# Kernel optimization log

Measured on AMD Instinct MI355X. Metric: run time of the kernel, lower is better.

The kernel has to match this reference:

```python
import jax, jax.numpy as jnp
import numpy as np

CURVATURE = -1.0
BN_EPS = 1e-5


def setup_inputs() -> dict:
    key = jax.random.key(0)
    k1, k2, k3 = jax.random.split(key, 3)
    B, Q, D, O = 4, 256, 256, 256  # Q must equal O for torch BatchNorm1d on 3D input
    x = jax.random.normal(k1, (B, Q, D), dtype=jnp.float32)
    # kaiming_uniform_(a=sqrt(5)) -> bound = 1/sqrt(fan_in)
    b_lc = 1.0 / np.sqrt(D * D)
    lc_w = jax.random.uniform(k2, (O, D, D), dtype=jnp.float32, minval=-b_lc, maxval=b_lc)
    b_w1 = 1.0 / np.sqrt(D)
    w1 = jax.random.uniform(k3, (O, D), dtype=jnp.float32, minval=-b_w1, maxval=b_w1)
    bias = jnp.zeros((O,), dtype=jnp.float32)
    gamma = jnp.ones((O,), dtype=jnp.float32)   # BN weight (channels = dim 1 = Q == O)
    beta = jnp.zeros((O,), dtype=jnp.float32)   # BN bias
    return {"x": x, "lc_w": lc_w, "w1": w1, "bias": bias, "gamma": gamma, "beta": beta}


def reference(x, lc_w, w1, bias, gamma, beta):
    B, Q, D = x.shape
    O = lc_w.shape[0]
    # pairwise products P[b,q,j,k] = x_j * x_k  (computed ONCE, shared across all i)
    P = x[:, :, :, None] * x[:, :, None, :]                     # [B,Q,D,D]
    # denom[b,j,k] = 1 + c * ||x[:,:,j]*x[:,:,k]||_2^2 over the query dim (dim=1)
    denom = 1.0 + CURVATURE * jnp.einsum('bqjk,bqjk->bjk', P, P)  # [B,D,D]
    # mask diagonal j==k in the weights (cheaper than masking P)
    mask = 1.0 - jnp.eye(D, dtype=x.dtype)
    Wm = lc_w * mask                                             # [O,D,D]
    lc_out = jnp.einsum('bqjk,ijk->bqi', P / denom[:, None, :, :], Wm)  # [B,Q,O]
    base = jnp.einsum('bqd,od->bqo', x, w1) + bias               # F.linear
    y = lc_out + base                                            # [B,Q,O]
    # BatchNorm1d(out_features) on 3D input: channels are dim 1 (requires Q == O),
    # training-mode batch stats over dims (0, 2), biased variance.
    mean = jnp.mean(y, axis=(0, 2), keepdims=True)
    var = jnp.mean((y - mean) ** 2, axis=(0, 2), keepdims=True)
    y_hat = (y - mean) / jnp.sqrt(var + BN_EPS)
    out = gamma[None, :, None] * y_hat + beta[None, :, None]
    # dropout treated as identity (eval mode) for a deterministic reference
    return out
```

## Files before the change

### kernel.cpp

```cpp
#include <hip/hip_runtime.h>
#include <hip/hip_bf16.h>

typedef __attribute__((ext_vector_type(8))) short short8;
typedef __attribute__((ext_vector_type(4))) float f32x4;
typedef __attribute__((ext_vector_type(4))) unsigned int u32x4;

#define LDP 40

static __device__ __forceinline__ unsigned int cvt_pk_bf16(float lo, float hi) {
    unsigned int r;
    asm("v_cvt_pk_bf16_f32 %0, %1, %2" : "=v"(r) : "v"(lo), "v"(hi));
    return r;
}

__global__ __launch_bounds__(256) void k_wcvt(const float* __restrict__ W,
                                              const float* __restrict__ w1,
                                              unsigned short* __restrict__ Wbf,
                                              unsigned short* __restrict__ w1bf) {
    long t0 = (long)blockIdx.x * 256 + threadIdx.x;
    for (long u = t0; u < 2097152L; u += 524288L) {
        long i = u >> 13;
        int uu = (int)(u & 8191);
        int c = uu >> 2, cu = uu & 3;
        int s = (int)((i >> 1) & 3);
        const float* src = W + i * 65536 + c * 32 + (cu ^ s) * 8;
        f32x4 a = *(const f32x4*)src;
        f32x4 b = *(const f32x4*)(src + 4);
        u32x4 q;
        q.x = cvt_pk_bf16(a.x, a.y); q.y = cvt_pk_bf16(a.z, a.w);
        q.z = cvt_pk_bf16(b.x, b.y); q.w = cvt_pk_bf16(b.z, b.w);
        *(u32x4*)(Wbf + u * 8) = q;
    }
    if (t0 < 8192) {
        long u = t0;
        long i = u >> 5;
        int uu = (int)(u & 31);
        int c = uu >> 2, cu = uu & 3;
        int s = (int)((i >> 1) & 3);
        const float* src = w1 + i * 256 + c * 32 + (cu ^ s) * 8;
        f32x4 a = *(const f32x4*)src;
        f32x4 b = *(const f32x4*)(src + 4);
        u32x4 q;
        q.x = cvt_pk_bf16(a.x, a.y); q.y = cvt_pk_bf16(a.z, a.w);
        q.z = cvt_pk_bf16(b.x, b.y); q.w = cvt_pk_bf16(b.z, b.w);
        *(u32x4*)(w1bf + u * 8) = q;
    }
}

__global__ __launch_bounds__(256) void k_pre(const float* __restrict__ x,
                                             float* __restrict__ T) {
    int bid = blockIdx.x, t = threadIdx.x;
    int b = bid >> 6;
    int j4 = (bid & 63) * 4;
    const float* xb = x + (long)b * 65536;
    float ac0 = 0.f, ac1 = 0.f, ac2 = 0.f, ac3 = 0.f;
    #pragma unroll 8
    for (int qq = 0; qq < 256; ++qq) {
        const float* row = xb + (long)qq * 256;
        float xk = row[t];
        float xk2 = xk * xk;
        f32x4 aj = *(const f32x4*)(row + j4);
        ac0 = fmaf(aj.x * aj.x, xk2, ac0);
        ac1 = fmaf(aj.y * aj.y, xk2, ac1);
        ac2 = fmaf(aj.z * aj.z, xk2, ac2);
        ac3 = fmaf(aj.w * aj.w, xk2, ac3);
    }
    long base = (long)b * 65536 + (long)j4 * 256 + t;
    T[base +   0] = (j4     == t) ? 0.f : 1.f / (1.f - ac0);
    T[base + 256] = (j4 + 1 == t) ? 0.f : 1.f / (1.f - ac1);
    T[base + 512] = (j4 + 2 == t) ? 0.f : 1.f / (1.f - ac2);
    T[base + 768] = (j4 + 3 == t) ? 0.f : 1.f / (1.f - ac3);
}

__global__ __launch_bounds__(256, 3) void k_gemm(const float* __restrict__ x,
                                                 const unsigned short* __restrict__ Wbf,
                                                 const unsigned short* __restrict__ w1bf,
                                                 const float* __restrict__ T,
                                                 float* __restrict__ partials) {
    __shared__ unsigned short As[2][128][LDP];
    __shared__ unsigned short Bs[2][128][32];

    const int bid = blockIdx.x;
    const int mt = bid >> 6;
    const int nt = (bid >> 5) & 1;
    const int sp = bid & 31;
    const int tid = threadIdx.x;
    const int lane = tid & 63;
    const int l15 = lane & 15;
    const int cu = lane >> 4;
    const int xu = cu ^ ((l15 >> 1) & 3);
    const int wid = tid >> 6;
    const int wm = wid >> 1, wn = wid & 1;
    const int b = mt >> 1;

    const int r = tid >> 1;
    const int ch = (tid & 1) * 16;

    const float* xrow = x + (long)(mt * 128 + r) * 256;
    const float* Trow = T + (long)b * 65536 + (long)(sp * 8) * 256 + ch;

    const unsigned short* Bsrc0 = Wbf + (long)(nt * 128 + wid * 32 + (lane >> 2)) * 65536
                                      + (long)sp * 2048 + (lane & 3) * 8;
    const unsigned short* Bsrc1 = Bsrc0 + 16L * 65536;

    f32x4 xjA = *(const f32x4*)(xrow + sp * 8);
    f32x4 xjB = *(const f32x4*)(xrow + sp * 8 + 4);
    const float xj8[8] = {xjA.x, xjA.y, xjA.z, xjA.w, xjB.x, xjB.y, xjB.z, xjB.w};

    f32x4 acc[4][4];
    #pragma unroll
    for (int a = 0; a < 4; ++a)
        #pragma unroll
        for (int c = 0; c < 4; ++c) acc[a][c] = (f32x4){0.f, 0.f, 0.f, 0.f};

    f32x4 xw0, xw1, xw2, xw3;

    {
        __builtin_amdgcn_global_load_lds(
            (const __attribute__((address_space(1))) unsigned int*)Bsrc0,
            (__attribute__((address_space(3))) unsigned int*)&Bs[0][wid * 32][0], 16, 0, 0);
        __builtin_amdgcn_global_load_lds(
            (const __attribute__((address_space(1))) unsigned int*)Bsrc1,
            (__attribute__((address_space(3))) unsigned int*)&Bs[0][wid * 32 + 16][0], 16, 0, 0);
        xw0 = *(const f32x4*)(xrow + ch + 0);
        xw1 = *(const f32x4*)(xrow + ch + 4);
        xw2 = *(const f32x4*)(xrow + ch + 8);
        xw3 = *(const f32x4*)(xrow + ch + 12);
        f32x4 t0 = *(const f32x4*)(Trow + 0);
        f32x4 t1 = *(const f32x4*)(Trow + 4);
        f32x4 t2 = *(const f32x4*)(Trow + 8);
        f32x4 t3 = *(const f32x4*)(Trow + 12);
        const float xj = xj8[0];
        u32x4 qa, qb;
        qa.x = cvt_pk_bf16(xj * xw0.x * t0.x, xj * xw0.y * t0.y);
        qa.y = cvt_pk_bf16(xj * xw0.z * t0.z, xj * xw0.w * t0.w);
        qa.z = cvt_pk_bf16(xj * xw1.x * t1.x, xj * xw1.y * t1.y);
        qa.w = cvt_pk_bf16(xj * xw1.z * t1.z, xj * xw1.w * t1.w);
        qb.x = cvt_pk_bf16(xj * xw2.x * t2.x, xj * xw2.y * t2.y);
        qb.y = cvt_pk_bf16(xj * xw2.z * t2.z, xj * xw2.w * t2.w);
        qb.z = cvt_pk_bf16(xj * xw3.x * t3.x, xj * xw3.y * t3.y);
        qb.w = cvt_pk_bf16(xj * xw3.z * t3.z, xj * xw3.w * t3.w);
        *(u32x4*)&As[0][r][ch]     = qa;
        *(u32x4*)&As[0][r][ch + 8] = qb;
    }
    __syncthreads();

    #pragma unroll 1
    for (int kw = 0; kw < 8; ++kw) {
        #pragma unroll
        for (int jj = 0; jj < 8; ++jj) {
            const int buf = jj & 1;
            const int nbuf = buf ^ 1;
            const int njj = (jj + 1) & 7;
            const int nkw = (jj == 7) ? kw + 1 : kw;
            const bool last = (jj == 7) && (kw == 7);

            f32x4 t0, t1, t2, t3;
            f32x4 nx0 = xw0, nx1 = xw1, nx2 = xw2, nx3 = xw3;
            if (!last) {
                const long noff = (long)njj * 256 + (long)nkw * 32;
                __builtin_amdgcn_global_load_lds(
                    (const __attribute__((address_space(1))) unsigned int*)(Bsrc0 + noff),
                    (__attribute__((address_space(3))) unsigned int*)&Bs[nbuf][wid * 32][0], 16, 0, 0);
                __builtin_amdgcn_global_load_lds(
                    (const __attribute__((address_space(1))) unsigned int*)(Bsrc1 + noff),
                    (__attribute__((address_space(3))) unsigned int*)&Bs[nbuf][wid * 32 + 16][0], 16, 0, 0);
                t0 = *(const f32x4*)(Trow + noff + 0);
                t1 = *(const f32x4*)(Trow + noff + 4);
                t2 = *(const f32x4*)(Trow + noff + 8);
                t3 = *(const f32x4*)(Trow + noff + 12);
                if (jj == 7) {
                    const long xo = (long)(kw + 1) * 32;
                    nx0 = *(const f32x4*)(xrow + xo + ch + 0);
                    nx1 = *(const f32x4*)(xrow + xo + ch + 4);
                    nx2 = *(const f32x4*)(xrow + xo + ch + 8);
                    nx3 = *(const f32x4*)(xrow + xo + ch + 12);
                }
            }

            short8 af[4], bfv[4];
            #pragma unroll
            for (int mf = 0; mf < 4; ++mf)
                af[mf] = *(const short8*)&As[buf][wm * 64 + mf * 16 + l15][cu * 8];
            #pragma unroll
            for (int nf = 0; nf < 4; ++nf)
                bfv[nf] = *(const short8*)((const char*)(&Bs[buf][0][0])
                            + (wn * 64 + nf * 16 + l15) * 64 + xu * 16);
            #pragma unroll
            for (int mf = 0; mf < 4; ++mf)
                #pragma unroll
                for (int nf = 0; nf < 4; ++nf)
                    acc[mf][nf] = __builtin_amdgcn_mfma_f32_16x16x32_bf16(
                        af[mf], bfv[nf], acc[mf][nf], 0, 0, 0);

            if (!last) {
                const float xjn = xj8[njj];
                u32x4 qa, qb;
                qa.x = cvt_pk_bf16(xjn * nx0.x * t0.x, xjn * nx0.y * t0.y);
                qa.y = cvt_pk_bf16(xjn * nx0.z * t0.z, xjn * nx0.w * t0.w);
                qa.z = cvt_pk_bf16(xjn * nx1.x * t1.x, xjn * nx1.y * t1.y);
                qa.w = cvt_pk_bf16(xjn * nx1.z * t1.z, xjn * nx1.w * t1.w);
                qb.x = cvt_pk_bf16(xjn * nx2.x * t2.x, xjn * nx2.y * t2.y);
                qb.y = cvt_pk_bf16(xjn * nx2.z * t2.z, xjn * nx2.w * t2.w);
                qb.z = cvt_pk_bf16(xjn * nx3.x * t3.x, xjn * nx3.y * t3.y);
                qb.w = cvt_pk_bf16(xjn * nx3.z * t3.z, xjn * nx3.w * t3.w);
                *(u32x4*)&As[nbuf][r][ch]     = qa;
                *(u32x4*)&As[nbuf][r][ch + 8] = qb;
            }
            __syncthreads();
            if (jj == 7) { xw0 = nx0; xw1 = nx1; xw2 = nx2; xw3 = nx3; }
        }
    }

    if (sp < 8) {
        const unsigned short* W1s = w1bf + (long)(nt * 128 + wid * 32 + (lane >> 2)) * 256
                                        + sp * 32 + (lane & 3) * 8;
        __builtin_amdgcn_global_load_lds(
            (const __attribute__((address_space(1))) unsigned int*)W1s,
            (__attribute__((address_space(3))) unsigned int*)&Bs[0][wid * 32][0], 16, 0, 0);
        __builtin_amdgcn_global_load_lds(
            (const __attribute__((address_space(1))) unsigned int*)(W1s + 16L * 256),
            (__attribute__((address_space(3))) unsigned int*)&Bs[0][wid * 32 + 16][0], 16, 0, 0);
        f32x4 a0 = *(const f32x4*)(xrow + sp * 32 + ch + 0);
        f32x4 a1 = *(const f32x4*)(xrow + sp * 32 + ch + 4);
        f32x4 a2 = *(const f32x4*)(xrow + sp * 32 + ch + 8);
        f32x4 a3 = *(const f32x4*)(xrow + sp * 32 + ch + 12);
        u32x4 qa, qb;
        qa.x = cvt_pk_bf16(a0.x, a0.y); qa.y = cvt_pk_bf16(a0.z, a0.w);
        qa.z = cvt_pk_bf16(a1.x, a1.y); qa.w = cvt_pk_bf16(a1.z, a1.w);
        qb.x = cvt_pk_bf16(a2.x, a2.y); qb.y = cvt_pk_bf16(a2.z, a2.w);
        qb.z = cvt_pk_bf16(a3.x, a3.y); qb.w = cvt_pk_bf16(a3.z, a3.w);
        *(u32x4*)&As[0][r][ch]     = qa;
        *(u32x4*)&As[0][r][ch + 8] = qb;
        __syncthreads();
        short8 af[4], bfv[4];
        #pragma unroll
        for (int mf = 0; mf < 4; ++mf)
            af[mf] = *(const short8*)&As[0][wm * 64 + mf * 16 + l15][cu * 8];
        #pragma unroll
        for (int nf = 0; nf < 4; ++nf)
            bfv[nf] = *(const short8*)((const char*)(&Bs[0][0][0])
                        + (wn * 64 + nf * 16 + l15) * 64 + xu * 16);
        #pragma unroll
        for (int mf = 0; mf < 4; ++mf)
            #pragma unroll
            for (int nf = 0; nf < 4; ++nf)
                acc[mf][nf] = __builtin_amdgcn_mfma_f32_16x16x32_bf16(
                    af[mf], bfv[nf], acc[mf][nf], 0, 0, 0);
    }

    float* Pp = partials + (long)sp * 262144;
    #pragma unroll
    for (int mf = 0; mf < 4; ++mf) {
        int rowb = mt * 128 + wm * 64 + mf * 16 + (lane >> 4) * 4;
        #pragma unroll
        for (int nf = 0; nf < 4; ++nf) {
            int col = nt * 128 + wn * 64 + nf * 16 + l15;
            #pragma unroll
            for (int rr = 0; rr < 4; ++rr)
                Pp[(long)(rowb + rr) * 256 + col] = acc[mf][nf][rr];
        }
    }
}

__global__ __launch_bounds__(256) void k_sum(const float* __restrict__ partials,
                                             const float* __restrict__ bias,
                                             float* __restrict__ y,
                                             float2* __restrict__ bstats) {
    int m = blockIdx.x;
    int o = threadIdx.x;
    float acc = bias[o];
    #pragma unroll 8
    for (int spi = 0; spi < 32; ++spi)
        acc += partials[((long)spi * 1024 + m) * 256 + o];
    y[(long)m * 256 + o] = acc;

    float s = acc, s2 = acc * acc;
    #pragma unroll
    for (int off = 32; off > 0; off >>= 1) {
        s  += __shfl_down(s, off, 64);
        s2 += __shfl_down(s2, off, 64);
    }
    __shared__ float rs[4], rq[4];
    int lane = o & 63, wv = o >> 6;
    if (lane == 0) { rs[wv] = s; rq[wv] = s2; }
    __syncthreads();
    if (o == 0) {
        float2 st;
        st.x = rs[0] + rs[1] + rs[2] + rs[3];
        st.y = rq[0] + rq[1] + rq[2] + rq[3];
        bstats[m] = st;
    }
}

__global__ __launch_bounds__(256) void k_bn(const float* __restrict__ y,
                                            const float2* __restrict__ bstats,
                                            const float* __restrict__ gamma,
                                            const float* __restrict__ beta,
                                            float* __restrict__ out) {
    int m = blockIdx.x;
    int o = threadIdx.x;
    int q = m & 255;
    float2 s0 = bstats[q], s1 = bstats[256 + q], s2 = bstats[512 + q], s3 = bstats[768 + q];
    float ts = s0.x + s1.x + s2.x + s3.x;
    float tq = s0.y + s1.y + s2.y + s3.y;
    float mean = ts * (1.f / 1024.f);
    float var = tq * (1.f / 1024.f) - mean * mean;
    float rstd = rsqrtf(var + 1e-5f);
    float v = y[(long)m * 256 + o];
    out[(long)m * 256 + o] = fmaf((v - mean) * rstd, gamma[q], beta[q]);
}

extern "C" void kernel_launch(void* const* d_in, const int* in_sizes, int n_in,
                              void* d_out, int out_size, void* d_ws, size_t ws_size,
                              hipStream_t stream) {
    const float* x     = (const float*)d_in[0];
    const float* lc_w  = (const float*)d_in[1];
    const float* w1    = (const float*)d_in[2];
    const float* bias  = (const float*)d_in[3];
    const float* gamma = (const float*)d_in[4];
    const float* beta  = (const float*)d_in[5];
    float* out = (float*)d_out;

    char* ws = (char*)d_ws;
    size_t o_T     = 0;
    size_t o_part  = o_T + 1048576;
    size_t o_y     = o_part + 33554432;
    size_t o_bst   = o_y + 1048576;
    size_t o_Wbf   = o_bst + 8192;
    size_t o_w1bf  = o_Wbf + 33554432;

    float*          T        = (float*)(ws + o_T);
    float*          partials = (float*)(ws + o_part);
    float*          y        = (float*)(ws + o_y);
    float2*         bstats   = (float2*)(ws + o_bst);
    unsigned short* Wbf      = (unsigned short*)(ws + o_Wbf);
    unsigned short* w1bf     = (unsigned short*)(ws + o_w1bf);

    k_wcvt<<<2048, 256, 0, stream>>>(lc_w, w1, Wbf, w1bf);
    k_pre <<<256,  256, 0, stream>>>(x, T);
    k_gemm<<<512,  256, 0, stream>>>(x, Wbf, w1bf, T, partials);
    k_sum <<<1024, 256, 0, stream>>>(partials, bias, y, bstats);
    k_bn  <<<1024, 256, 0, stream>>>(y, bstats, gamma, beta, out);
}
```

Baseline: 204.8 us.

## Triple-buffer B tiles with vmcnt-based barriers, swizzle A in LDS, merge prep kernels

The GEMM main loop now prefetches B tiles two steps ahead into a three-slot LDS ring. It replaces __syncthreads with a partial s_waitcnt vmcnt barrier so global-to-LDS loads stay in flight across iterations. The A tile drops its padded stride in favour of an XOR swizzle matching the read pattern, and the T scale loads are software-pipelined one step ahead. The weight-conversion and denominator kernels are fused into one launch, and the GEMM's launch bounds drop to two blocks per CU, which risks lower occupancy in exchange for more registers.

```diff
diff --git a/kernel.cpp b/kernel.cpp
--- a/kernel.cpp
+++ b/kernel.cpp
@@ -4,8 +4,6 @@
 typedef __attribute__((ext_vector_type(8))) short short8;
 typedef __attribute__((ext_vector_type(4))) float f32x4;
 typedef __attribute__((ext_vector_type(4))) unsigned int u32x4;
-
-#define LDP 40
 
 static __device__ __forceinline__ unsigned int cvt_pk_bf16(float lo, float hi) {
     unsigned int r;
@@ -13,72 +11,84 @@
     return r;
 }
 
-__global__ __launch_bounds__(256) void k_wcvt(const float* __restrict__ W,
+#define GLDS(src, dst) __builtin_amdgcn_global_load_lds( \
+    (const __attribute__((address_space(1))) unsigned int*)(src), \
+    (__attribute__((address_space(3))) unsigned int*)(dst), 16, 0, 0)
+
+#define BARC(N) do { \
+    asm volatile("s_waitcnt lgkmcnt(0) vmcnt(" #N ")" ::: "memory"); \
+    __builtin_amdgcn_s_barrier(); \
+    __builtin_amdgcn_sched_barrier(0); \
+} while (0)
+
+__global__ __launch_bounds__(256) void k_prep(const float* __restrict__ x,
+                                              const float* __restrict__ W,
                                               const float* __restrict__ w1,
                                               unsigned short* __restrict__ Wbf,
-                                              unsigned short* __restrict__ w1bf) {
-    long t0 = (long)blockIdx.x * 256 + threadIdx.x;
-    for (long u = t0; u < 2097152L; u += 524288L) {
-        long i = u >> 13;
-        int uu = (int)(u & 8191);
-        int c = uu >> 2, cu = uu & 3;
-        int s = (int)((i >> 1) & 3);
-        const float* src = W + i * 65536 + c * 32 + (cu ^ s) * 8;
-        f32x4 a = *(const f32x4*)src;
-        f32x4 b = *(const f32x4*)(src + 4);
-        u32x4 q;
-        q.x = cvt_pk_bf16(a.x, a.y); q.y = cvt_pk_bf16(a.z, a.w);
-        q.z = cvt_pk_bf16(b.x, b.y); q.w = cvt_pk_bf16(b.z, b.w);
-        *(u32x4*)(Wbf + u * 8) = q;
-    }
-    if (t0 < 8192) {
-        long u = t0;
-        long i = u >> 5;
-        int uu = (int)(u & 31);
-        int c = uu >> 2, cu = uu & 3;
-        int s = (int)((i >> 1) & 3);
-        const float* src = w1 + i * 256 + c * 32 + (cu ^ s) * 8;
-        f32x4 a = *(const f32x4*)src;
-        f32x4 b = *(const f32x4*)(src + 4);
-        u32x4 q;
-        q.x = cvt_pk_bf16(a.x, a.y); q.y = cvt_pk_bf16(a.z, a.w);
-        q.z = cvt_pk_bf16(b.x, b.y); q.w = cvt_pk_bf16(b.z, b.w);
-        *(u32x4*)(w1bf + u * 8) = q;
-    }
-}
-
-__global__ __launch_bounds__(256) void k_pre(const float* __restrict__ x,
-                                             float* __restrict__ T) {
+                                              unsigned short* __restrict__ w1bf,
+                                              float* __restrict__ T) {
     int bid = blockIdx.x, t = threadIdx.x;
-    int b = bid >> 6;
-    int j4 = (bid & 63) * 4;
-    const float* xb = x + (long)b * 65536;
-    float ac0 = 0.f, ac1 = 0.f, ac2 = 0.f, ac3 = 0.f;
-    #pragma unroll 8
-    for (int qq = 0; qq < 256; ++qq) {
-        const float* row = xb + (long)qq * 256;
-        float xk = row[t];
-        float xk2 = xk * xk;
-        f32x4 aj = *(const f32x4*)(row + j4);
-        ac0 = fmaf(aj.x * aj.x, xk2, ac0);
-        ac1 = fmaf(aj.y * aj.y, xk2, ac1);
-        ac2 = fmaf(aj.z * aj.z, xk2, ac2);
-        ac3 = fmaf(aj.w * aj.w, xk2, ac3);
-    }
-    long base = (long)b * 65536 + (long)j4 * 256 + t;
-    T[base +   0] = (j4     == t) ? 0.f : 1.f / (1.f - ac0);
-    T[base + 256] = (j4 + 1 == t) ? 0.f : 1.f / (1.f - ac1);
-    T[base + 512] = (j4 + 2 == t) ? 0.f : 1.f / (1.f - ac2);
-    T[base + 768] = (j4 + 3 == t) ? 0.f : 1.f / (1.f - ac3);
-}
-
-__global__ __launch_bounds__(256, 3) void k_gemm(const float* __restrict__ x,
+    if (bid < 2048) {
+        long t0 = (long)bid * 256 + t;
+        for (long u = t0; u < 2097152L; u += 524288L) {
+            long i = u >> 13;
+            int uu = (int)(u & 8191);
+            int c = uu >> 2, cu = uu & 3;
+            int s = (int)((i >> 1) & 3);
+            const float* src = W + i * 65536 + c * 32 + (cu ^ s) * 8;
+            f32x4 a = *(const f32x4*)src;
+            f32x4 b = *(const f32x4*)(src + 4);
+            u32x4 q;
+            q.x = cvt_pk_bf16(a.x, a.y); q.y = cvt_pk_bf16(a.z, a.w);
+            q.z = cvt_pk_bf16(b.x, b.y); q.w = cvt_pk_bf16(b.z, b.w);
+            *(u32x4*)(Wbf + u * 8) = q;
+        }
+        if (t0 < 8192) {
+            long u = t0;
+            long i = u >> 5;
+            int uu = (int)(u & 31);
+            int c = uu >> 2, cu = uu & 3;
+            int s = (int)((i >> 1) & 3);
+            const float* src = w1 + i * 256 + c * 32 + (cu ^ s) * 8;
+            f32x4 a = *(const f32x4*)src;
+            f32x4 b = *(const f32x4*)(src + 4);
+            u32x4 q;
+            q.x = cvt_pk_bf16(a.x, a.y); q.y = cvt_pk_bf16(a.z, a.w);
+            q.z = cvt_pk_bf16(b.x, b.y); q.w = cvt_pk_bf16(b.z, b.w);
+            *(u32x4*)(w1bf + u * 8) = q;
+        }
+    } else {
+        int bb = bid - 2048;
+        int b = bb >> 6;
+        int j4 = (bb & 63) * 4;
+        const float* xb = x + (long)b * 65536;
+        float ac0 = 0.f, ac1 = 0.f, ac2 = 0.f, ac3 = 0.f;
+        #pragma unroll 8
+        for (int qq = 0; qq < 256; ++qq) {
+            const float* row = xb + (long)qq * 256;
+            float xk = row[t];
+            float xk2 = xk * xk;
+            f32x4 aj = *(const f32x4*)(row + j4);
+            ac0 = fmaf(aj.x * aj.x, xk2, ac0);
+            ac1 = fmaf(aj.y * aj.y, xk2, ac1);
+            ac2 = fmaf(aj.z * aj.z, xk2, ac2);
+            ac3 = fmaf(aj.w * aj.w, xk2, ac3);
+        }
+        long base = (long)b * 65536 + (long)j4 * 256 + t;
+        T[base +   0] = (j4     == t) ? 0.f : 1.f / (1.f - ac0);
+        T[base + 256] = (j4 + 1 == t) ? 0.f : 1.f / (1.f - ac1);
+        T[base + 512] = (j4 + 2 == t) ? 0.f : 1.f / (1.f - ac2);
+        T[base + 768] = (j4 + 3 == t) ? 0.f : 1.f / (1.f - ac3);
+    }
+}
+
+__global__ __launch_bounds__(256, 2) void k_gemm(const float* __restrict__ x,
                                                  const unsigned short* __restrict__ Wbf,
                                                  const unsigned short* __restrict__ w1bf,
                                                  const float* __restrict__ T,
                                                  float* __restrict__ partials) {
-    __shared__ unsigned short As[2][128][LDP];
-    __shared__ unsigned short Bs[2][128][32];
+    __shared__ unsigned short As[2][128][32];
+    __shared__ unsigned short Bs[3][128][32];
 
     const int bid = blockIdx.x;
     const int mt = bid >> 6;
@@ -95,6 +105,10 @@
 
     const int r = tid >> 1;
     const int ch = (tid & 1) * 16;
+    const int u0 = ch >> 3;
+    const int sAr = (r >> 1) & 3;
+    const int wcol0 = ((u0 ^ sAr) * 8);
+    const int wcol1 = (((u0 + 1) ^ sAr) * 8);
 
     const float* xrow = x + (long)(mt * 128 + r) * 256;
     const float* Trow = T + (long)b * 65536 + (long)(sp * 8) * 256 + ch;
@@ -114,14 +128,15 @@
         for (int c = 0; c < 4; ++c) acc[a][c] = (f32x4){0.f, 0.f, 0.f, 0.f};
 
     f32x4 xw0, xw1, xw2, xw3;
+    f32x4 tn0, tn1, tn2, tn3;
+    unsigned short* const As0 = &As[0][0][0];
+    unsigned short* const Bs0 = &Bs[0][0][0];
 
     {
-        __builtin_amdgcn_global_load_lds(
-            (const __attribute__((address_space(1))) unsigned int*)Bsrc0,
-            (__attribute__((address_space(3))) unsigned int*)&Bs[0][wid * 32][0], 16, 0, 0);
-        __builtin_amdgcn_global_load_lds(
-            (const __attribute__((address_space(1))) unsigned int*)Bsrc1,
-            (__attribute__((address_space(3))) unsigned int*)&Bs[0][wid * 32 + 16][0], 16, 0, 0);
+        GLDS(Bsrc0, Bs0 + (long)(wid * 32) * 32);
+        GLDS(Bsrc1, Bs0 + (long)(wid * 32 + 16) * 32);
+        GLDS(Bsrc0 + 256, Bs0 + 4096 + (long)(wid * 32) * 32);
+        GLDS(Bsrc1 + 256, Bs0 + 4096 + (long)(wid * 32 + 16) * 32);
         xw0 = *(const f32x4*)(xrow + ch + 0);
         xw1 = *(const f32x4*)(xrow + ch + 4);
         xw2 = *(const f32x4*)(xrow + ch + 8);
@@ -130,6 +145,10 @@
         f32x4 t1 = *(const f32x4*)(Trow + 4);
         f32x4 t2 = *(const f32x4*)(Trow + 8);
         f32x4 t3 = *(const f32x4*)(Trow + 12);
+        tn0 = *(const f32x4*)(Trow + 256 + 0);
+        tn1 = *(const f32x4*)(Trow + 256 + 4);
+        tn2 = *(const f32x4*)(Trow + 256 + 8);
+        tn3 = *(const f32x4*)(Trow + 256 + 12);
         const float xj = xj8[0];
         u32x4 qa, qb;
         qa.x = cvt_pk_bf16(xj * xw0.x * t0.x, xj * xw0.y * t0.y);
@@ -140,52 +159,67 @@
         qb.y = cvt_pk_bf16(xj * xw2.z * t2.z, xj * xw2.w * t2.w);
         qb.z = cvt_pk_bf16(xj * xw3.x * t3.x, xj * xw3.y * t3.y);
         qb.w = cvt_pk_bf16(xj * xw3.z * t3.z, xj * xw3.w * t3.w);
-        *(u32x4*)&As[0][r][ch]     = qa;
-        *(u32x4*)&As[0][r][ch + 8] = qb;
+        *(u32x4*)(As0 + (long)r * 32 + wcol0) = qa;
+        *(u32x4*)(As0 + (long)r * 32 + wcol1) = qb;
     }
     __syncthreads();
 
+    int b0 = 0;
     #pragma unroll 1
     for (int kw = 0; kw < 8; ++kw) {
+        f32x4 nx0, nx1, nx2, nx3;
         #pragma unroll
         for (int jj = 0; jj < 8; ++jj) {
-            const int buf = jj & 1;
-            const int nbuf = buf ^ 1;
-            const int njj = (jj + 1) & 7;
-            const int nkw = (jj == 7) ? kw + 1 : kw;
-            const bool last = (jj == 7) && (kw == 7);
-
-            f32x4 t0, t1, t2, t3;
-            f32x4 nx0 = xw0, nx1 = xw1, nx2 = xw2, nx3 = xw3;
-            if (!last) {
-                const long noff = (long)njj * 256 + (long)nkw * 32;
-                __builtin_amdgcn_global_load_lds(
-                    (const __attribute__((address_space(1))) unsigned int*)(Bsrc0 + noff),
-                    (__attribute__((address_space(3))) unsigned int*)&Bs[nbuf][wid * 32][0], 16, 0, 0);
-                __builtin_amdgcn_global_load_lds(
-                    (const __attribute__((address_space(1))) unsigned int*)(Bsrc1 + noff),
-                    (__attribute__((address_space(3))) unsigned int*)&Bs[nbuf][wid * 32 + 16][0], 16, 0, 0);
-                t0 = *(const f32x4*)(Trow + noff + 0);
-                t1 = *(const f32x4*)(Trow + noff + 4);
-                t2 = *(const f32x4*)(Trow + noff + 8);
-                t3 = *(const f32x4*)(Trow + noff + 12);
-                if (jj == 7) {
-                    const long xo = (long)(kw + 1) * 32;
-                    nx0 = *(const f32x4*)(xrow + xo + ch + 0);
-                    nx1 = *(const f32x4*)(xrow + xo + ch + 4);
-                    nx2 = *(const f32x4*)(xrow + xo + ch + 8);
-                    nx3 = *(const f32x4*)(xrow + xo + ch + 12);
-                }
+            int rb = b0 + (jj % 3); rb = rb >= 3 ? rb - 3 : rb;
+            int wb = rb + 2; wb = wb >= 3 ? wb - 3 : wb;
+            const int cbuf = jj & 1;
+            const int nbuf = cbuf ^ 1;
+
+            const int nkw2 = kw + ((jj + 2) >> 3);
+            const long off2 = (long)((jj + 2) & 7) * 256 + (long)nkw2 * 32;
+            GLDS(Bsrc0 + off2, Bs0 + (long)wb * 4096 + (long)(wid * 32) * 32);
+            GLDS(Bsrc1 + off2, Bs0 + (long)wb * 4096 + (long)(wid * 32 + 16) * 32);
+            f32x4 tf0 = *(const f32x4*)(Trow + off2 + 0);
+            f32x4 tf1 = *(const f32x4*)(Trow + off2 + 4);
+            f32x4 tf2 = *(const f32x4*)(Trow + off2 + 8);
+            f32x4 tf3 = *(const f32x4*)(Trow + off2 + 12);
+            if (jj == 6) {
+                const long xo = (kw == 7) ? 0 : (long)(kw + 1) * 32;
+                nx0 = *(const f32x4*)(xrow + xo + ch + 0);
+                nx1 = *(const f32x4*)(xrow + xo + ch + 4);
+                nx2 = *(const f32x4*)(xrow + xo + ch + 8);
+                nx3 = *(const f32x4*)(xrow + xo + ch + 12);
             }
 
             short8 af[4], bfv[4];
             #pragma unroll
             for (int mf = 0; mf < 4; ++mf)
-                af[mf] = *(const short8*)&As[buf][wm * 64 + mf * 16 + l15][cu * 8];
+                af[mf] = *(const short8*)(As0 + (long)cbuf * 4096
+                            + (long)(wm * 64 + mf * 16 + l15) * 32 + xu * 8);
             #pragma unroll
             for (int nf = 0; nf < 4; ++nf)
-                bfv[nf] = *(const short8*)((const char*)(&Bs[buf][0][0])
-                            + (wn * 64 + nf * 16 + l15) * 64 + xu * 16);
+                bfv[nf] = *(const short8*)(Bs0 + (long)rb * 4096
+                            + (long)(wn * 64 + nf * 16 + l15) * 32 + xu * 8);
+
+            {
+                const float xjn = xj8[(jj + 1) & 7];
+                const f32x4 w0 = (jj == 7) ? nx0 : xw0;
+                const f32x4 w1v = (jj == 7) ? nx1 : xw1;
+                const f32x4 w2 = (jj == 7) ? nx2 : xw2;
+                const f32x4 w3 = (jj == 7) ? nx3 : xw3;
+                u32x4 qa, qb;
+                qa.x = cvt_pk_bf16(xjn * w0.x * tn0.x, xjn * w0.y * tn0.y);
+                qa.y = cvt_pk_bf16(xjn * w0.z * tn0.z, xjn * w0.w * tn0.w);
+                qa.z = cvt_pk_bf16(xjn * w1v.x * tn1.x, xjn * w1v.y * tn1.y);
+                qa.w = cvt_pk_bf16(xjn * w1v.z * tn1.z, xjn * w1v.w * tn1.w);
+                qb.x = cvt_pk_bf16(xjn * w2.x * tn2.x, xjn * w2.y * tn2.y);
+                qb.y = cvt_pk_bf16(xjn * w2.z * tn2.z, xjn * w2.w * tn2.w);
+                qb.z = cvt_pk_bf16(xjn * w3.x * tn3.x, xjn * w3.y * tn3.y);
+                qb.w = cvt_pk_bf16(xjn * w3.z * tn3.z, xjn * w3.w * tn3.w);
+                *(u32x4*)(As0 + (long)nbuf * 4096 + (long)r * 32 + wcol0) = qa;
+                *(u32x4*)(As0 + (long)nbuf * 4096 + (long)r * 32 + wcol1) = qb;
+            }
+
             #pragma unroll
             for (int mf = 0; mf < 4; ++mf)
                 #pragma unroll
@@ -193,34 +227,20 @@
                     acc[mf][nf] = __builtin_amdgcn_mfma_f32_16x16x32_bf16(
                         af[mf], bfv[nf], acc[mf][nf], 0, 0, 0);
 
-            if (!last) {
-                const float xjn = xj8[njj];
-                u32x4 qa, qb;
-                qa.x = cvt_pk_bf16(xjn * nx0.x * t0.x, xjn * nx0.y * t0.y);
-                qa.y = cvt_pk_bf16(xjn * nx0.z * t0.z, xjn * nx0.w * t0.w);
-                qa.z = cvt_pk_bf16(xjn * nx1.x * t1.x, xjn * nx1.y * t1.y);
-                qa.w = cvt_pk_bf16(xjn * nx1.z * t1.z, xjn * nx1.w * t1.w);
-                qb.x = cvt_pk_bf16(xjn * nx2.x * t2.x, xjn * nx2.y * t2.y);
-                qb.y = cvt_pk_bf16(xjn * nx2.z * t2.z, xjn * nx2.w * t2.w);
-                qb.z = cvt_pk_bf16(xjn * nx3.x * t3.x, xjn * nx3.y * t3.y);
-                qb.w = cvt_pk_bf16(xjn * nx3.z * t3.z, xjn * nx3.w * t3.w);
-                *(u32x4*)&As[nbuf][r][ch]     = qa;
-                *(u32x4*)&As[nbuf][r][ch + 8] = qb;
-            }
-            __syncthreads();
+            tn0 = tf0; tn1 = tf1; tn2 = tf2; tn3 = tf3;
             if (jj == 7) { xw0 = nx0; xw1 = nx1; xw2 = nx2; xw3 = nx3; }
-        }
-    }
-
+
+            if (jj == 6 || jj == 7) { BARC(12); } else { BARC(8); }
+        }
+        b0 += 2; if (b0 >= 3) b0 -= 3;
+    }
+
+    __syncthreads();
     if (sp < 8) {
         const unsigned short* W1s = w1bf + (long)(nt * 128 + wid * 32 + (lane >> 2)) * 256
                                         + sp * 32 + (lane & 3) * 8;
-        __builtin_amdgcn_global_load_lds(
-            (const __attribute__((address_space(1))) unsigned int*)W1s,
-            (__attribute__((address_space(3))) unsigned int*)&Bs[0][wid * 32][0], 16, 0, 0);
-        __builtin_amdgcn_global_load_lds(
-            (const __attribute__((address_space(1))) unsigned int*)(W1s + 16L * 256),
-            (__attribute__((address_space(3))) unsigned int*)&Bs[0][wid * 32 + 16][0], 16, 0, 0);
+        GLDS(W1s, Bs0 + (long)(wid * 32) * 32);
+        GLDS(W1s + 16L * 256, Bs0 + (long)(wid * 32 + 16) * 32);
         f32x4 a0 = *(const f32x4*)(xrow + sp * 32 + ch + 0);
         f32x4 a1 = *(const f32x4*)(xrow + sp * 32 + ch + 4);
         f32x4 a2 = *(const f32x4*)(xrow + sp * 32 + ch + 8);
@@ -230,17 +250,16 @@
         qa.z = cvt_pk_bf16(a1.x, a1.y); qa.w = cvt_pk_bf16(a1.z, a1.w);
         qb.x = cvt_pk_bf16(a2.x, a2.y); qb.y = cvt_pk_bf16(a2.z, a2.w);
         qb.z = cvt_pk_bf16(a3.x, a3.y); qb.w = cvt_pk_bf16(a3.z, a3.w);
-        *(u32x4*)&As[0][r][ch]     = qa;
-        *(u32x4*)&As[0][r][ch + 8] = qb;
+        *(u32x4*)(As0 + (long)r * 32 + wcol0) = qa;
+        *(u32x4*)(As0 + (long)r * 32 + wcol1) = qb;
         __syncthreads();
         short8 af[4], bfv[4];
         #pragma unroll
         for (int mf = 0; mf < 4; ++mf)
-            af[mf] = *(const short8*)&As[0][wm * 64 + mf * 16 + l15][cu * 8];
+            af[mf] = *(const short8*)(As0 + (long)(wm * 64 + mf * 16 + l15) * 32 + xu * 8);
         #pragma unroll
         for (int nf = 0; nf < 4; ++nf)
-            bfv[nf] = *(const short8*)((const char*)(&Bs[0][0][0])
-                        + (wn * 64 + nf * 16 + l15) * 64 + xu * 16);
+            bfv[nf] = *(const short8*)(Bs0 + (long)(wn * 64 + nf * 16 + l15) * 32 + xu * 8);
         #pragma unroll
         for (int mf = 0; mf < 4; ++mf)
             #pragma unroll
@@ -337,8 +356,7 @@
     unsigned short* Wbf      = (unsigned short*)(ws + o_Wbf);
     unsigned short* w1bf     = (unsigned short*)(ws + o_w1bf);
 
-    k_wcvt<<<2048, 256, 0, stream>>>(lc_w, w1, Wbf, w1bf);
-    k_pre <<<256,  256, 0, stream>>>(x, T);
+    k_prep<<<2304, 256, 0, stream>>>(x, lc_w, w1, Wbf, w1bf, T);
     k_gemm<<<512,  256, 0, stream>>>(x, Wbf, w1bf, T, partials);
     k_sum <<<1024, 256, 0, stream>>>(partials, bias, y, bstats);
     k_bn  <<<1024, 256, 0, stream>>>(y, bstats, gamma, beta, out);
```

Result: faster. 185.3 us (-9.5%).
